# Optimization experiments

Measured on AMD Instinct MI355X. Metric: run time of the kernel, lower is better.

The kernel has to match this reference:

```python
import jax, jax.numpy as jnp
import numpy as np

EPS = 1e-5
MAG_EPS = 1e-12  # guards sqrt grad at exactly 0


def _conv(x, w, b, pad):
    # x: NCHW, w: OIHW, stride 1, symmetric padding -> SAME for odd kernels
    y = jax.lax.conv_general_dilated(x, w, (1, 1), [(pad, pad), (pad, pad)],
                                     dimension_numbers=('NCHW', 'OIHW', 'NCHW'))
    return y + b[None, :, None, None]


def _cconv(xr, xi, wr, wi, br, bi, pad):
    # apply_complex: (conv_r(xr) - conv_i(xi)) + j(conv_r(xi) + conv_i(xr)), biases inside each real conv
    yr = _conv(xr, wr, br, pad) - _conv(xi, wi, bi, pad)
    yi = _conv(xi, wr, br, pad) + _conv(xr, wi, bi, pad)
    return yr, yi


def _cbn(xr, xi, grr, gri, gii, br, bi):
    # complex batch norm with 2x2 covariance whitening (training-mode batch stats)
    ax = (0, 2, 3)
    bc = lambda v: v[None, :, None, None]
    cr = xr - bc(xr.mean(ax))
    ci = xi - bc(xi.mean(ax))
    Crr = (cr * cr).mean(ax) + EPS
    Cii = (ci * ci).mean(ax) + EPS
    Cri = (cr * ci).mean(ax)
    s = jnp.sqrt(Crr * Cii - Cri * Cri)          # sqrt(det)
    t = jnp.sqrt(Crr + Cii + 2.0 * s)            # sqrt(trace + 2 sqrt(det))
    inv = 1.0 / (s * t)
    Rrr, Rii, Rri = (Cii + s) * inv, (Crr + s) * inv, -Cri * inv
    xhr = bc(Rrr) * cr + bc(Rri) * ci
    xhi = bc(Rri) * cr + bc(Rii) * ci
    yr = bc(grr) * xhr + bc(gri) * xhi + bc(br)
    yi = bc(gri) * xhr + bc(gii) * xhi + bc(bi)
    return yr, yi


def _crelu(xr, xi):
    return jnp.maximum(xr, 0.0), jnp.maximum(xi, 0.0)


def _cmaxpool2(xr, xi):
    # 2x2 max pool selecting the complex value with the largest magnitude
    N, C, H, W = xr.shape
    blk = lambda x: x.reshape(N, C, H // 2, 2, W // 2, 2).transpose(0, 1, 2, 4, 3, 5).reshape(N, C, H // 2, W // 2, 4)
    br_, bi_ = blk(xr), blk(xi)
    idx = jnp.argmax(br_ * br_ + bi_ * bi_, axis=-1, keepdims=True)
    yr = jnp.take_along_axis(br_, idx, axis=-1)[..., 0]
    yi = jnp.take_along_axis(bi_, idx, axis=-1)[..., 0]
    return yr, yi


def _net(x,
         c1_wr, c1_wi, c1_br, c1_bi, b1_grr, b1_gri, b1_gii, b1_br, b1_bi,
         c2_wr, c2_wi, c2_br, c2_bi, b2_grr, b2_gri, b2_gii, b2_br, b2_bi,
         c3_wr, c3_wi, c3_br, c3_bi, b3_grr, b3_gri, b3_gii, b3_br, b3_bi,
         c4_wr, c4_wi, c4_br, c4_bi, b4_grr, b4_gri, b4_gii, b4_br, b4_bi,
         fc1_wr, fc1_wi, fc1_br, fc1_bi, fc2_w, fc2_b):
    # conv1: input has zero imaginary part, so the complex conv folds into two real convs
    xr = _conv(x, c1_wr, c1_br - c1_bi, 5)
    xi = _conv(x, c1_wi, c1_br + c1_bi, 5)
    xr, xi = _cmaxpool2(*_crelu(*_cbn(xr, xi, b1_grr, b1_gri, b1_gii, b1_br, b1_bi)))
    xr, xi = _cconv(xr, xi, c2_wr, c2_wi, c2_br, c2_bi, 2)
    xr, xi = _cmaxpool2(*_crelu(*_cbn(xr, xi, b2_grr, b2_gri, b2_gii, b2_br, b2_bi)))
    xr, xi = _cconv(xr, xi, c3_wr, c3_wi, c3_br, c3_bi, 1)
    xr, xi = _cmaxpool2(*_crelu(*_cbn(xr, xi, b3_grr, b3_gri, b3_gii, b3_br, b3_bi)))
    xr, xi = _cconv(xr, xi, c4_wr, c4_wi, c4_br, c4_bi, 1)
    xr, xi = _cmaxpool2(*_crelu(*_cbn(xr, xi, b4_grr, b4_gri, b4_gii, b4_br, b4_bi)))
    N = xr.shape[0]
    fr, fi = xr.reshape(N, -1), xi.reshape(N, -1)  # (N, 1024)
    er = (fr @ fc1_wr.T + fc1_br) - (fi @ fc1_wi.T + fc1_bi)
    ei = (fi @ fc1_wr.T + fc1_br) + (fr @ fc1_wi.T + fc1_bi)
    er, ei = jnp.maximum(er, 0.0), jnp.maximum(ei, 0.0)  # complex relu
    mag = jnp.sqrt(er * er + ei * ei + MAG_EPS)          # |z|; dropout is identity at eval
    logits = mag @ fc2_w.T + fc2_b
    return logits, er, ei


def setup_inputs() -> dict:
    key = jax.random.key(0)
    ks = iter(jax.random.split(key, 64))
    d = {}
    d['x'] = jax.random.normal(next(ks), (512, 1, 64, 64), jnp.float32)
    for name, cin, cout, k in [('c1', 1, 16, 11), ('c2', 16, 32, 5), ('c3', 32, 64, 3), ('c4', 64, 64, 3)]:
        s = 1.0 / np.sqrt(cin * k * k)
        d[f'{name}_wr'] = jax.random.normal(next(ks), (cout, cin, k, k), jnp.float32) * s
        d[f'{name}_wi'] = jax.random.normal(next(ks), (cout, cin, k, k), jnp.float32) * s
        d[f'{name}_br'] = jax.random.normal(next(ks), (cout,), jnp.float32) * s
        d[f'{name}_bi'] = jax.random.normal(next(ks), (cout,), jnp.float32) * s
    for name, c in [('b1', 16), ('b2', 32), ('b3', 64), ('b4', 64)]:
        d[f'{name}_grr'] = jnp.full((c,), 1.0 / np.sqrt(2.0), jnp.float32)
        d[f'{name}_gri'] = jnp.zeros((c,), jnp.float32)
        d[f'{name}_gii'] = jnp.full((c,), 1.0 / np.sqrt(2.0), jnp.float32)
        d[f'{name}_br'] = jnp.zeros((c,), jnp.float32)
        d[f'{name}_bi'] = jnp.zeros((c,), jnp.float32)
    s = 1.0 / np.sqrt(1024.0)
    d['fc1_wr'] = jax.random.normal(next(ks), (256, 1024), jnp.float32) * s
    d['fc1_wi'] = jax.random.normal(next(ks), (256, 1024), jnp.float32) * s
    d['fc1_br'] = jax.random.normal(next(ks), (256,), jnp.float32) * s
    d['fc1_bi'] = jax.random.normal(next(ks), (256,), jnp.float32) * s
    d['fc2_w'] = jax.random.normal(next(ks), (1000, 256), jnp.float32) * (1.0 / 16.0)
    d['fc2_b'] = jnp.zeros((1000,), jnp.float32)
    return d


def reference(x,
              c1_wr, c1_wi, c1_br, c1_bi, b1_grr, b1_gri, b1_gii, b1_br, b1_bi,
              c2_wr, c2_wi, c2_br, c2_bi, b2_grr, b2_gri, b2_gii, b2_br, b2_bi,
              c3_wr, c3_wi, c3_br, c3_bi, b3_grr, b3_gri, b3_gii, b3_br, b3_bi,
              c4_wr, c4_wi, c4_br, c4_bi, b4_grr, b4_gri, b4_gii, b4_br, b4_bi,
              fc1_wr, fc1_wi, fc1_br, fc1_bi, fc2_w, fc2_b):
    # returns (logits, emb_real, emb_imag); torch returned complex embeddings, split here into real pairs
    return _net(x,
                c1_wr, c1_wi, c1_br, c1_bi, b1_grr, b1_gri, b1_gii, b1_br, b1_bi,
                c2_wr, c2_wi, c2_br, c2_bi, b2_grr, b2_gri, b2_gii, b2_br, b2_bi,
                c3_wr, c3_wi, c3_br, c3_bi, b3_grr, b3_gri, b3_gii, b3_br, b3_bi,
                c4_wr, c4_wi, c4_br, c4_bi, b4_grr, b4_gri, b4_gii, b4_br, b4_bi,
                fc1_wr, fc1_wi, fc1_br, fc1_bi, fc2_w, fc2_b)
```

## Files before the change

### kernel.cpp

```cpp
#include <hip/hip_runtime.h>
#include <math.h>

__global__ __launch_bounds__(256) void fill_kernel(float* p, int n, float v) {
  int i = blockIdx.x * 256 + threadIdx.x;
  if (i < n) p[i] = v;
}

__device__ __forceinline__ void bn_apply_f32(float xr, float xi,
                                             const float* __restrict__ cf,
                                             float grr, float gri, float gii,
                                             float bbr, float bbi, float& yr,
                                             float& yi) {
  float cr = __fsub_rn(xr, cf[0]);
  float ci = __fsub_rn(xi, cf[1]);
  float xhr = __fadd_rn(__fmul_rn(cf[2], cr), __fmul_rn(cf[4], ci));
  float xhi = __fadd_rn(__fmul_rn(cf[4], cr), __fmul_rn(cf[3], ci));
  yr = fmaxf(__fadd_rn(__fadd_rn(__fmul_rn(grr, xhr), __fmul_rn(gri, xhi)), bbr), 0.f);
  yi = fmaxf(__fadd_rn(__fadd_rn(__fmul_rn(gri, xhr), __fmul_rn(gii, xhi)), bbi), 0.f);
}

#define PFMA8(XX, YY, WV1, WV2) \
  XX = fmaf(v4.x, WV1.x, XX);   \
  XX = fmaf(v4.y, WV1.y, XX);   \
  XX = fmaf(v4.z, WV1.z, XX);   \
  XX = fmaf(v4.w, WV1.w, XX);   \
  YY = fmaf(v4.x, WV2.x, YY);   \
  YY = fmaf(v4.y, WV2.y, YY);   \
  YY = fmaf(v4.z, WV2.z, YY);   \
  YY = fmaf(v4.w, WV2.w, YY);

#define C1_ROWBASE(pr) ((pr) * 84 + (((pr) >> 1) & 1))

template <int PASS>
__global__ __launch_bounds__(256, 2) void conv1_stats2(
    const float* __restrict__ x, const float* __restrict__ wr,
    const float* __restrict__ wi, const float* __restrict__ br,
    const float* __restrict__ bi, const float* __restrict__ coef,
    float* __restrict__ partial) {
  int b = blockIdx.x;
  int n = b >> 2, cg = b & 3;
  int t = threadIdx.x;
  __shared__ __align__(16) float sx[74 * 84];
  __shared__ __align__(16) float4 swr4[121], swi4[121];
  __shared__ float s0[256], s1[256], s2[PASS ? 256 : 1];

  for (int i = t; i < 74 * 84; i += 256) sx[i] = 0.f;
  for (int idx = t; idx < 484; idx += 256) {
    int wo = idx >> 2, ci = idx & 3;
    ((float*)swr4)[idx] = wr[(size_t)(cg * 4 + ci) * 121 + wo];
    ((float*)swi4)[idx] = wi[(size_t)(cg * 4 + ci) * 121 + wo];
  }
  __syncthreads();
  const float* xn = x + (size_t)n * 4096;
  for (int idx = t; idx < 1024; idx += 256) {
    float4 v = *(const float4*)(xn + idx * 4);
    int iy = idx >> 4, ixb = (idx & 15) * 4;
    int base = C1_ROWBASE(iy + 5) + ixb + 5;
    sx[base + 0] = v.x; sx[base + 1] = v.y;
    sx[base + 2] = v.z; sx[base + 3] = v.w;
  }
  __syncthreads();

  int leaf = t >> 3, j = t & 7;
  float a[4][16], bb[4][16];
#pragma unroll
  for (int ci = 0; ci < 4; ++ci)
#pragma unroll
    for (int k = 0; k < 16; ++k) { a[ci][k] = 0.f; bb[ci][k] = 0.f; }

  for (int ky = 0; ky < 11; ++ky) {
    int pr0 = leaf * 2 + ky;
    int base0 = C1_ROWBASE(pr0) + j;
    int base1 = C1_ROWBASE(pr0 + 1) + j;
    for (int kx = 0; kx < 11; ++kx) {
      const float* tb0 = sx + base0 + kx;
      const float* tb1 = sx + base1 + kx;
      float4 wR = swr4[ky * 11 + kx];
      float4 wI = swi4[ky * 11 + kx];
#pragma unroll
      for (int k8 = 0; k8 < 8; ++k8) {
        float v = tb0[k8 * 8];
        a[0][k8] = fmaf(v, wR.x, a[0][k8]);  bb[0][k8] = fmaf(v, wI.x, bb[0][k8]);
        a[1][k8] = fmaf(v, wR.y, a[1][k8]);  bb[1][k8] = fmaf(v, wI.y, bb[1][k8]);
        a[2][k8] = fmaf(v, wR.z, a[2][k8]);  bb[2][k8] = fmaf(v, wI.z, bb[2][k8]);
        a[3][k8] = fmaf(v, wR.w, a[3][k8]);  bb[3][k8] = fmaf(v, wI.w, bb[3][k8]);
      }
#pragma unroll
      for (int k8 = 0; k8 < 8; ++k8) {
        float v = tb1[k8 * 8];
        a[0][8 + k8] = fmaf(v, wR.x, a[0][8 + k8]);  bb[0][8 + k8] = fmaf(v, wI.x, bb[0][8 + k8]);
        a[1][8 + k8] = fmaf(v, wR.y, a[1][8 + k8]);  bb[1][8 + k8] = fmaf(v, wI.y, bb[1][8 + k8]);
        a[2][8 + k8] = fmaf(v, wR.z, a[2][8 + k8]);  bb[2][8 + k8] = fmaf(v, wI.z, bb[2][8 + k8]);
        a[3][8 + k8] = fmaf(v, wR.w, a[3][8 + k8]);  bb[3][8 + k8] = fmaf(v, wI.w, bb[3][8 + k8]);
      }
    }
  }

#pragma unroll
  for (int ci = 0; ci < 4; ++ci) {
    int c = cg * 4 + ci;
    float addR = __fsub_rn(br[c], bi[c]);
    float addI = __fadd_rn(br[c], bi[c]);
    float mr = 0.f, mi = 0.f;
    if (PASS) { mr = coef[c * 5 + 0]; mi = coef[c * 5 + 1]; }
    float a0 = 0.f, a1 = 0.f, a2 = 0.f;
#pragma unroll
    for (int k = 0; k < 16; ++k) {
      float xr = __fadd_rn(a[ci][k], addR);
      float xi = __fadd_rn(bb[ci][k], addI);
      if (PASS == 0) {
        a0 = __fadd_rn(a0, xr);
        a1 = __fadd_rn(a1, xi);
      } else {
        float cr = __fsub_rn(xr, mr), ci2 = __fsub_rn(xi, mi);
        a0 = __fadd_rn(a0, __fmul_rn(cr, cr));
        a1 = __fadd_rn(a1, __fmul_rn(ci2, ci2));
        a2 = __fadd_rn(a2, __fmul_rn(cr, ci2));
      }
    }
    s0[t] = a0; s1[t] = a1; if (PASS) s2[t] = a2;
    __syncthreads();
    if (t < 32) {
      int o = t * 8;
      float v0 = __fadd_rn(__fadd_rn(__fadd_rn(s0[o], s0[o + 1]), __fadd_rn(s0[o + 2], s0[o + 3])),
                           __fadd_rn(__fadd_rn(s0[o + 4], s0[o + 5]), __fadd_rn(s0[o + 6], s0[o + 7])));
      float v1 = __fadd_rn(__fadd_rn(__fadd_rn(s1[o], s1[o + 1]), __fadd_rn(s1[o + 2], s1[o + 3])),
                           __fadd_rn(__fadd_rn(s1[o + 4], s1[o + 5]), __fadd_rn(s1[o + 6], s1[o + 7])));
      float v2 = 0.f;
      if (PASS)
        v2 = __fadd_rn(__fadd_rn(__fadd_rn(s2[o], s2[o + 1]), __fadd_rn(s2[o + 2], s2[o + 3])),
                       __fadd_rn(__fadd_rn(s2[o + 4], s2[o + 5]), __fadd_rn(s2[o + 6], s2[o + 7])));
      s0[t] = v0; s1[t] = v1; if (PASS) s2[t] = v2;
    }
    if (t == 0) {
      for (int wdt = 32; wdt > 1; wdt >>= 1)
        for (int i = 0; i < (wdt >> 1); ++i) {
          s0[i] = __fadd_rn(s0[2 * i], s0[2 * i + 1]);
          s1[i] = __fadd_rn(s1[2 * i], s1[2 * i + 1]);
          if (PASS) s2[i] = __fadd_rn(s2[2 * i], s2[2 * i + 1]);
        }
      constexpr int S = PASS ? 3 : 2;
      size_t base = ((size_t)(n * 16 + c)) * S;
      partial[base + 0] = s0[0];
      partial[base + 1] = s1[0];
      if (PASS) partial[base + 2] = s2[0];
    }
    __syncthreads();
  }
}

__global__ __launch_bounds__(256, 2) void conv1_pool2(
    const float* __restrict__ x, const float* __restrict__ wr,
    const float* __restrict__ wi, const float* __restrict__ br,
    const float* __restrict__ bi, const float* __restrict__ coef,
    const float* __restrict__ grr, const float* __restrict__ gri,
    const float* __restrict__ gii, const float* __restrict__ bbr,
    const float* __restrict__ bbi, float* __restrict__ Pr,
    float* __restrict__ Pi) {
  int b = blockIdx.x;
  int n = b >> 2, cg = b & 3;
  int t = threadIdx.x;
  __shared__ __align__(16) float sx[74 * 84];
  __shared__ __align__(16) float4 swr4[121], swi4[121];

  for (int i = t; i < 74 * 84; i += 256) sx[i] = 0.f;
  for (int idx = t; idx < 484; idx += 256) {
    int wo = idx >> 2, ci = idx & 3;
    ((float*)swr4)[idx] = wr[(size_t)(cg * 4 + ci) * 121 + wo];
    ((float*)swi4)[idx] = wi[(size_t)(cg * 4 + ci) * 121 + wo];
  }
  __syncthreads();
  const float* xn = x + (size_t)n * 4096;
  for (int idx = t; idx < 1024; idx += 256) {
    float4 v = *(const float4*)(xn + idx * 4);
    int iy = idx >> 4, ixb = (idx & 15) * 4;
    int base = C1_ROWBASE(iy + 5) + ixb + 5;
    sx[base + 0] = v.x; sx[base + 1] = v.y;
    sx[base + 2] = v.z; sx[base + 3] = v.w;
  }
  __syncthreads();

  int oyb = t >> 5, ox = t & 31;
  float A[4][16], Bb[4][16];
#pragma unroll
  for (int ci = 0; ci < 4; ++ci)
#pragma unroll
    for (int e = 0; e < 16; ++e) { A[ci][e] = 0.f; Bb[ci][e] = 0.f; }

  for (int ky = 0; ky < 11; ++ky) {
    for (int kx = 0; kx < 11; ++kx) {
      float4 wR = swr4[ky * 11 + kx];
      float4 wI = swi4[ky * 11 + kx];
#pragma unroll
      for (int e = 0; e < 16; ++e) {
        int i = e >> 2, p = e & 3;
        int pr = 2 * (oyb + i * 8) + (p >> 1) + ky;
        int pc = 2 * ox + (p & 1) + kx;
        float v = sx[C1_ROWBASE(pr) + pc];
        A[0][e] = fmaf(v, wR.x, A[0][e]);  Bb[0][e] = fmaf(v, wI.x, Bb[0][e]);
        A[1][e] = fmaf(v, wR.y, A[1][e]);  Bb[1][e] = fmaf(v, wI.y, Bb[1][e]);
        A[2][e] = fmaf(v, wR.z, A[2][e]);  Bb[2][e] = fmaf(v, wI.z, Bb[2][e]);
        A[3][e] = fmaf(v, wR.w, A[3][e]);  Bb[3][e] = fmaf(v, wI.w, Bb[3][e]);
      }
    }
  }

#pragma unroll
  for (int ci = 0; ci < 4; ++ci) {
    int c = cg * 4 + ci;
    float addR = __fsub_rn(br[c], bi[c]);
    float addI = __fadd_rn(br[c], bi[c]);
    const float* cf = coef + c * 5;
    float gR = grr[c], gI = gri[c], gG = gii[c], bR = bbr[c], bI2 = bbi[c];
#pragma unroll
    for (int i = 0; i < 4; ++i) {
      int oy = oyb + i * 8;
      float bestr = 0.f, besti = 0.f, bestm = -1.f;
#pragma unroll
      for (int p = 0; p < 4; ++p) {
        float xr = __fadd_rn(A[ci][i * 4 + p], addR);
        float xi = __fadd_rn(Bb[ci][i * 4 + p], addI);
        float yr, yi;
        bn_apply_f32(xr, xi, cf, gR, gI, gG, bR, bI2, yr, yi);
        float m = __fadd_rn(__fmul_rn(yr, yr), __fmul_rn(yi, yi));
        if (m > bestm) { bestm = m; bestr = yr; besti = yi; }
      }
      size_t o = ((size_t)(n * 16 + c) * 32 + oy) * 32 + ox;
      Pr[o] = bestr;
      Pi[o] = besti;
    }
  }
}

__global__ __launch_bounds__(256) void repack_w(const float* __restrict__ src,
                                                float* __restrict__ dst,
                                                int CIN, int KK, int total) {
  int i = blockIdx.x * 256 + threadIdx.x;
  if (i >= total) return;
  int kk = i % KK;
  int rem = i / KK;
  int ci = rem % CIN;
  int co = rem / CIN;
  dst[((size_t)co * KK + kk) * CIN + ci] = src[i];
}

__global__ __launch_bounds__(256) void transpose_rc(const float* __restrict__ src,
                                                    float* __restrict__ dst,
                                                    int R, int C) {
  int i = blockIdx.x * 256 + threadIdx.x;
  if (i >= R * C) return;
  int r = i / C, c = i % C;
  dst[(size_t)c * R + r] = src[i];
}

#define STAGE_COMP(SRCBASE)                                          \
  {                                                                  \
    const float* src_ = (SRCBASE) + (size_t)n * CIN * HH;            \
    for (int idx = t; idx < RALLOC * H * CINQ; idx += NT) {          \
      int px = idx % (RALLOC * H);                                   \
      int cq = idx / (RALLOC * H);                                   \
      int lr = px / H, col = px - lr * H;                            \
      int gr = r0 + lr;                                              \
      if (gr < 0 || gr >= H) continue;                               \
      const float* sp = src_ + (size_t)cq * 4 * HH + gr * H + col;   \
      float4 v;                                                      \
      v.x = sp[0]; v.y = sp[HH]; v.z = sp[2 * HH]; v.w = sp[3 * HH]; \
      *(float4*)&sin_[(lr * W + col + PAD) * ST1 + cq * 4] = v;      \
    }                                                                \
  }

template <int H, int CIN, int COUT, int K, int PASS>
__global__ __launch_bounds__(COUT * 4, 2) void cconv_band_stats(
    const float* __restrict__ Xr, const float* __restrict__ Xi,
    const float* __restrict__ wrT, const float* __restrict__ wiT,
    const float* __restrict__ br, const float* __restrict__ bi,
    const float* __restrict__ coef, float* __restrict__ partial) {
  constexpr int HH = H * H;
  constexpr int PAD = K / 2, KK = K * K;
  constexpr int CLEN = (HH >= 128) ? 16 : 8;
  constexpr int NLEAF = HH / (8 * CLEN);
  constexpr int BROWS = (CLEN * 8) / H;
  constexpr int RALLOC = BROWS + 2 * PAD;
  constexpr int W = H + 2 * PAD;
  constexpr int ST1 = CIN + 4;
  constexpr int CINQ = CIN / 4;
  constexpr int NT = COUT * 4;
  constexpr int NC = COUT * 8;

  __shared__ __align__(16) float sin_[RALLOC * W * ST1];
  __shared__ float red0[NC], red1[NC], red2[PASS ? NC : 1];

  int b = blockIdx.x;
  int leaf = b % NLEAF;
  int n = b / NLEAF;
  int t = threadIdx.x;
  int r0 = leaf * BROWS - PAD;

  for (int i = t; i < RALLOC * W * ST1; i += NT) sin_[i] = 0.f;
  __syncthreads();
  STAGE_COMP(Xr)
  __syncthreads();

  int c0 = t >> 3, j = t & 7;
  int c1 = c0 + COUT / 2;
  const float* wrb0 = wrT + (size_t)c0 * CIN * KK;
  const float* wib0 = wiT + (size_t)c0 * CIN * KK;
  const float* wrb1 = wrT + (size_t)c1 * CIN * KK;
  const float* wib1 = wiT + (size_t)c1 * CIN * KK;

  float A0[CLEN], D0[CLEN], A1[CLEN], D1[CLEN];
  float B0[CLEN], C0_[CLEN], B1[CLEN], C1_[CLEN];
#pragma unroll
  for (int k = 0; k < CLEN; ++k) {
    A0[k] = 0.f; D0[k] = 0.f; A1[k] = 0.f; D1[k] = 0.f;
    B0[k] = 0.f; C0_[k] = 0.f; B1[k] = 0.f; C1_[k] = 0.f;
  }

#define STATS_TAPS(PH)                                                        \
  for (int ky = 0; ky < K; ++ky) {                                            \
    for (int kx = 0; kx < K; ++kx) {                                          \
      const float* tb = sin_ + (ky * W + kx + j) * ST1;                       \
      const float* wrp0 = wrb0 + (ky * K + kx) * CIN;                         \
      const float* wip0 = wib0 + (ky * K + kx) * CIN;                         \
      const float* wrp1 = wrb1 + (ky * K + kx) * CIN;                         \
      const float* wip1 = wib1 + (ky * K + kx) * CIN;                         \
      _Pragma("unroll 2") for (int cq = 0; cq < CINQ; ++cq) {                 \
        const float* tbc = tb + cq * 4;                                       \
        float4 wR0v = *(const float4*)(wrp0 + cq * 4);                        \
        float4 wI0v = *(const float4*)(wip0 + cq * 4);                        \
        float4 wR1v = *(const float4*)(wrp1 + cq * 4);                        \
        float4 wI1v = *(const float4*)(wip1 + cq * 4);                        \
        _Pragma("unroll") for (int k = 0; k < CLEN; ++k) {                    \
          float4 v4 = *(const float4*)(tbc +                                  \
              (((k * 8) / H) * W + ((k * 8) % H)) * ST1);                     \
          if (PH == 0) {                                                      \
            PFMA8(A0[k], D0[k], wR0v, wI0v)                                   \
            PFMA8(A1[k], D1[k], wR1v, wI1v)                                   \
          } else {                                                            \
            PFMA8(B0[k], C0_[k], wI0v, wR0v)                                  \
            PFMA8(B1[k], C1_[k], wI1v, wR1v)                                  \
          }                                                                   \
        }                                                                     \
      }                                                                       \
    }                                                                         \
  }

  STATS_TAPS(0)
  __syncthreads();
  STAGE_COMP(Xi)
  __syncthreads();
  STATS_TAPS(1)
#undef STATS_TAPS

  {
    float cbR = br[c0], cbI = bi[c0];
    float mr = 0.f, mi = 0.f;
    if (PASS) { mr = coef[c0 * 5 + 0]; mi = coef[c0 * 5 + 1]; }
    float a0 = 0.f, a1 = 0.f, a2 = 0.f;
#pragma unroll
    for (int k = 0; k < CLEN; ++k) {
      float yr = __fsub_rn(__fadd_rn(A0[k], cbR), __fadd_rn(B0[k], cbI));
      float yi = __fadd_rn(__fadd_rn(C0_[k], cbR), __fadd_rn(D0[k], cbI));
      if (PASS == 0) {
        a0 = __fadd_rn(a0, yr);
        a1 = __fadd_rn(a1, yi);
      } else {
        float cr = __fsub_rn(yr, mr), ci = __fsub_rn(yi, mi);
        a0 = __fadd_rn(a0, __fmul_rn(cr, cr));
        a1 = __fadd_rn(a1, __fmul_rn(ci, ci));
        a2 = __fadd_rn(a2, __fmul_rn(cr, ci));
      }
    }
    red0[c0 * 8 + j] = a0; red1[c0 * 8 + j] = a1;
    if (PASS) red2[c0 * 8 + j] = a2;
  }
  {
    float cbR = br[c1], cbI = bi[c1];
    float mr = 0.f, mi = 0.f;
    if (PASS) { mr = coef[c1 * 5 + 0]; mi = coef[c1 * 5 + 1]; }
    float a0 = 0.f, a1 = 0.f, a2 = 0.f;
#pragma unroll
    for (int k = 0; k < CLEN; ++k) {
      float yr = __fsub_rn(__fadd_rn(A1[k], cbR), __fadd_rn(B1[k], cbI));
      float yi = __fadd_rn(__fadd_rn(C1_[k], cbR), __fadd_rn(D1[k], cbI));
      if (PASS == 0) {
        a0 = __fadd_rn(a0, yr);
        a1 = __fadd_rn(a1, yi);
      } else {
        float cr = __fsub_rn(yr, mr), ci = __fsub_rn(yi, mi);
        a0 = __fadd_rn(a0, __fmul_rn(cr, cr));
        a1 = __fadd_rn(a1, __fmul_rn(ci, ci));
        a2 = __fadd_rn(a2, __fmul_rn(cr, ci));
      }
    }
    red0[c1 * 8 + j] = a0; red1[c1 * 8 + j] = a1;
    if (PASS) red2[c1 * 8 + j] = a2;
  }
  __syncthreads();
  if (j == 0) {
    constexpr int S = PASS ? 3 : 2;
#pragma unroll
    for (int s = 0; s < 2; ++s) {
      int cc = s ? c1 : c0;
      int o = cc * 8;
      size_t base = (((size_t)n * COUT + cc) * NLEAF + leaf) * S;
      partial[base + 0] =
          __fadd_rn(__fadd_rn(__fadd_rn(red0[o], red0[o + 1]), __fadd_rn(red0[o + 2], red0[o + 3])),
                    __fadd_rn(__fadd_rn(red0[o + 4], red0[o + 5]), __fadd_rn(red0[o + 6], red0[o + 7])));
      partial[base + 1] =
          __fadd_rn(__fadd_rn(__fadd_rn(red1[o], red1[o + 1]), __fadd_rn(red1[o + 2], red1[o + 3])),
                    __fadd_rn(__fadd_rn(red1[o + 4], red1[o + 5]), __fadd_rn(red1[o + 6], red1[o + 7])));
      if (PASS)
        partial[base + 2] =
            __fadd_rn(__fadd_rn(__fadd_rn(red2[o], red2[o + 1]), __fadd_rn(red2[o + 2], red2[o + 3])),
                      __fadd_rn(__fadd_rn(red2[o + 4], red2[o + 5]), __fadd_rn(red2[o + 6], red2[o + 7])));
    }
  }
}

template <int H, int CIN, int COUT, int K, int OBR>
__global__ __launch_bounds__(COUT * 4, 2) void cconv_band_pool(
    const float* __restrict__ Xr, const float* __restrict__ Xi,
    const float* __restrict__ wrT, const float* __restrict__ wiT,
    const float* __restrict__ br, const float* __restrict__ bi,
    const float* __restrict__ coef, const float* __restrict__ grr,
    const float* __restrict__ gri, const float* __restrict__ gii,
    const float* __restrict__ bbr, const float* __restrict__ bbi,
    float* __restrict__ Pr, float* __restrict__ Pi) {
  constexpr int HH = H * H;
  constexpr int OH = H / 2;
  constexpr int NBAND = OH / OBR;
  constexpr int PAD = K / 2, KK = K * K;
  constexpr int CROWS = OBR * 2;
  constexpr int RALLOC = CROWS + 2 * PAD;
  constexpr int W = H + 2 * PAD;
  constexpr int ST1 = CIN + 4;
  constexpr int CINQ = CIN / 4;
  constexpr int NT = COUT * 4;
  constexpr int NOUT = (OBR * OH) / 8;
  constexpr int NQ = NOUT * 4;

  __shared__ __align__(16) float sin_[RALLOC * W * ST1];

  int b = blockIdx.x;
  int band = b % NBAND;
  int n = b / NBAND;
  int t = threadIdx.x;
  int r0 = band * CROWS - PAD;

  for (int i = t; i < RALLOC * W * ST1; i += NT) sin_[i] = 0.f;
  __syncthreads();
  STAGE_COMP(Xr)
  __syncthreads();

  int c0 = t >> 3, j = t & 7;
  int c1 = c0 + COUT / 2;
  const float* jbp = sin_ + (2 * (j / OH) * W + 2 * (j % OH)) * ST1;
  const float* wrb0 = wrT + (size_t)c0 * CIN * KK;
  const float* wib0 = wiT + (size_t)c0 * CIN * KK;
  const float* wrb1 = wrT + (size_t)c1 * CIN * KK;
  const float* wib1 = wiT + (size_t)c1 * CIN * KK;

  float A0[NQ], D0[NQ], A1[NQ], D1[NQ];
  float B0[NQ], C0_[NQ], B1[NQ], C1_[NQ];
#pragma unroll
  for (int q = 0; q < NQ; ++q) {
    A0[q] = 0.f; D0[q] = 0.f; A1[q] = 0.f; D1[q] = 0.f;
    B0[q] = 0.f; C0_[q] = 0.f; B1[q] = 0.f; C1_[q] = 0.f;
  }

#define POOL_TAPS(PH)                                                         \
  for (int ky = 0; ky < K; ++ky) {                                            \
    for (int kx = 0; kx < K; ++kx) {                                          \
      const float* tb = jbp + (ky * W + kx) * ST1;                            \
      const float* wrp0 = wrb0 + (ky * K + kx) * CIN;                         \
      const float* wip0 = wib0 + (ky * K + kx) * CIN;                         \
      const float* wrp1 = wrb1 + (ky * K + kx) * CIN;                         \
      const float* wip1 = wib1 + (ky * K + kx) * CIN;                         \
      _Pragma("unroll 2") for (int cq = 0; cq < CINQ; ++cq) {                 \
        const float* tbc = tb + cq * 4;                                       \
        float4 wR0v = *(const float4*)(wrp0 + cq * 4);                        \
        float4 wI0v = *(const float4*)(wip0 + cq * 4);                        \
        float4 wR1v = *(const float4*)(wrp1 + cq * 4);                        \
        float4 wI1v = *(const float4*)(wip1 + cq * 4);                        \
        _Pragma("unroll") for (int q = 0; q < NQ; ++q) {                      \
          float4 v4 = *(const float4*)(tbc +                                  \
              ((2 * ((8 * (q >> 2)) / OH) + ((q & 3) >> 1)) * W +             \
               2 * ((8 * (q >> 2)) % OH) + ((q & 3) & 1)) * ST1);             \
          if (PH == 0) {                                                      \
            PFMA8(A0[q], D0[q], wR0v, wI0v)                                   \
            PFMA8(A1[q], D1[q], wR1v, wI1v)                                   \
          } else {                                                            \
            PFMA8(B0[q], C0_[q], wI0v, wR0v)                                  \
            PFMA8(B1[q], C1_[q], wI1v, wR1v)                                  \
          }                                                                   \
        }                                                                     \
      }                                                                       \
    }                                                                         \
  }

  POOL_TAPS(0)
  __syncthreads();
  STAGE_COMP(Xi)
  __syncthreads();
  POOL_TAPS(1)
#undef POOL_TAPS

  {
    float cbR = br[c0], cbI = bi[c0];
    const float* cf = coef + c0 * 5;
    float gR = grr[c0], gI = gri[c0], gG = gii[c0], bR = bbr[c0], bI2 = bbi[c0];
#pragma unroll
    for (int u = 0; u < NOUT; ++u) {
      int e = j + 8 * u;
      int oy = band * OBR + e / OH, ox = e % OH;
      float bestr = 0.f, besti = 0.f, bestm = -1.f;
#pragma unroll
      for (int p = 0; p < 4; ++p) {
        int q = u * 4 + p;
        float xr = __fsub_rn(__fadd_rn(A0[q], cbR), __fadd_rn(B0[q], cbI));
        float xi = __fadd_rn(__fadd_rn(C0_[q], cbR), __fadd_rn(D0[q], cbI));
        float yr, yi;
        bn_apply_f32(xr, xi, cf, gR, gI, gG, bR, bI2, yr, yi);
        float m = __fadd_rn(__fmul_rn(yr, yr), __fmul_rn(yi, yi));
        if (m > bestm) { bestm = m; bestr = yr; besti = yi; }
      }
      size_t o = ((size_t)(n * COUT + c0) * OH + oy) * OH + ox;
      Pr[o] = bestr;
      Pi[o] = besti;
    }
  }
  {
    float cbR = br[c1], cbI = bi[c1];
    const float* cf = coef + c1 * 5;
    float gR = grr[c1], gI = gri[c1], gG = gii[c1], bR = bbr[c1], bI2 = bbi[c1];
#pragma unroll
    for (int u = 0; u < NOUT; ++u) {
      int e = j + 8 * u;
      int oy = band * OBR + e / OH, ox = e % OH;
      float bestr = 0.f, besti = 0.f, bestm = -1.f;
#pragma unroll
      for (int p = 0; p < 4; ++p) {
        int q = u * 4 + p;
        float xr = __fsub_rn(__fadd_rn(A1[q], cbR), __fadd_rn(B1[q], cbI));
        float xi = __fadd_rn(__fadd_rn(C1_[q], cbR), __fadd_rn(D1[q], cbI));
        float yr, yi;
        bn_apply_f32(xr, xi, cf, gR, gI, gG, bR, bI2, yr, yi);
        float m = __fadd_rn(__fmul_rn(yr, yr), __fmul_rn(yi, yi));
        if (m > bestm) { bestm = m; bestr = yr; besti = yi; }
      }
      size_t o = ((size_t)(n * COUT + c1) * OH + oy) * OH + ox;
      Pr[o] = bestr;
      Pi[o] = besti;
    }
  }
}

template <int H, int CIN, int COUT, int CG, int K, int REPS>
__global__ __launch_bounds__((CG / 2) * 8 * REPS, 2) void cconv_band_store(
    const float* __restrict__ Xr, const float* __restrict__ Xi,
    const float* __restrict__ wrT, const float* __restrict__ wiT,
    const float* __restrict__ br, const float* __restrict__ bi,
    int coff, float* __restrict__ bufR, float* __restrict__ bufI) {
  constexpr int HH = H * H;
  constexpr int PAD = K / 2, KK = K * K;
  constexpr int CLEN = (HH >= 128) ? 16 : 8;
  constexpr int NLEAF = HH / (8 * CLEN);
  constexpr int BROWS = (CLEN * 8) / H;
  constexpr int RALLOC = BROWS + 2 * PAD;
  constexpr int W = H + 2 * PAD;
  constexpr int ST1 = CIN + 4;
  constexpr int CINQ = CIN / 4;
  constexpr int CPAIR = CG / 2;
  constexpr int NT = CPAIR * 8 * REPS;
  constexpr int CLT = CLEN / REPS;
  constexpr int RROWS = (CLT * 8) / H;

  __shared__ __align__(16) float sin_[RALLOC * W * ST1];

  int b = blockIdx.x;
  int leaf = b % NLEAF;
  int n = b / NLEAF;
  int t = threadIdx.x;
  int r0 = leaf * BROWS - PAD;

  for (int i = t; i < RALLOC * W * ST1; i += NT) sin_[i] = 0.f;
  __syncthreads();
  STAGE_COMP(Xr)
  __syncthreads();

  int rep = t / (CPAIR * 8);
  int tt = t % (CPAIR * 8);
  int c0l = tt >> 3, j = tt & 7;
  int c0 = coff + c0l, c1 = c0 + CPAIR;
  const float* jbp = sin_ + ((REPS > 1 ? rep * RROWS : 0) * W + j) * ST1;
  const float* wrb0 = wrT + (size_t)c0 * CIN * KK;
  const float* wib0 = wiT + (size_t)c0 * CIN * KK;
  const float* wrb1 = wrT + (size_t)c1 * CIN * KK;
  const float* wib1 = wiT + (size_t)c1 * CIN * KK;

  float A0[CLT], D0[CLT], A1[CLT], D1[CLT];
  float B0[CLT], C0_[CLT], B1[CLT], C1_[CLT];
#pragma unroll
  for (int k = 0; k < CLT; ++k) {
    A0[k] = 0.f; D0[k] = 0.f; A1[k] = 0.f; D1[k] = 0.f;
    B0[k] = 0.f; C0_[k] = 0.f; B1[k] = 0.f; C1_[k] = 0.f;
  }

#define STORE_TAPS(PH)                                                        \
  for (int ky = 0; ky < K; ++ky) {                                            \
    for (int kx = 0; kx < K; ++kx) {                                          \
      const float* tb = jbp + (ky * W + kx) * ST1;                            \
      const float* wrp0 = wrb0 + (ky * K + kx) * CIN;                         \
      const float* wip0 = wib0 + (ky * K + kx) * CIN;                         \
      const float* wrp1 = wrb1 + (ky * K + kx) * CIN;                         \
      const float* wip1 = wib1 + (ky * K + kx) * CIN;                         \
      _Pragma("unroll 2") for (int cq = 0; cq < CINQ; ++cq) {                 \
        const float* tbc = tb + cq * 4;                                       \
        float4 wR0v = *(const float4*)(wrp0 + cq * 4);                        \
        float4 wI0v = *(const float4*)(wip0 + cq * 4);                        \
        float4 wR1v = *(const float4*)(wrp1 + cq * 4);                        \
        float4 wI1v = *(const float4*)(wip1 + cq * 4);                        \
        _Pragma("unroll") for (int k = 0; k < CLT; ++k) {                     \
          float4 v4 = *(const float4*)(tbc +                                  \
              (((k * 8) / H) * W + ((k * 8) % H)) * ST1);                     \
          if (PH == 0) {                                                      \
            PFMA8(A0[k], D0[k], wR0v, wI0v)                                   \
            PFMA8(A1[k], D1[k], wR1v, wI1v)                                   \
          } else {                                                            \
            PFMA8(B0[k], C0_[k], wI0v, wR0v)                                  \
            PFMA8(B1[k], C1_[k], wI1v, wR1v)                                  \
          }                                                                   \
        }                                                                     \
      }                                                                       \
    }                                                                         \
  }

  STORE_TAPS(0)
  __syncthreads();
  STAGE_COMP(Xi)
  __syncthreads();
  STORE_TAPS(1)
#undef STORE_TAPS

  float cbR0 = br[c0], cbI0 = bi[c0];
  float cbR1 = br[c1], cbI1 = bi[c1];
  size_t b0 = ((size_t)n * CG + c0l) * HH;
  size_t b1 = ((size_t)n * CG + (c0l + CPAIR)) * HH;
#pragma unroll
  for (int k = 0; k < CLT; ++k) {
    int px = leaf * CLEN * 8 + (rep * CLT + k) * 8 + j;
    float yr0 = __fsub_rn(__fadd_rn(A0[k], cbR0), __fadd_rn(B0[k], cbI0));
    float yi0 = __fadd_rn(__fadd_rn(C0_[k], cbR0), __fadd_rn(D0[k], cbI0));
    bufR[b0 + px] = yr0;
    bufI[b0 + px] = yi0;
    float yr1 = __fsub_rn(__fadd_rn(A1[k], cbR1), __fadd_rn(B1[k], cbI1));
    float yi1 = __fadd_rn(__fadd_rn(C1_[k], cbR1), __fadd_rn(D1[k], cbI1));
    bufR[b1 + px] = yr1;
    bufI[b1 + px] = yi1;
  }
}

template <int CG, int HH, int CLEN, int PASS>
__global__ __launch_bounds__(CG * 8) void cstats_stream(
    const float* __restrict__ bufR, const float* __restrict__ bufI,
    const float* __restrict__ coef, float* __restrict__ partial, int coff) {
  constexpr int NLEAF = HH / (8 * CLEN);
  constexpr int NT = CG * 8;
  __shared__ float red0[NT], red1[NT], red2[PASS ? NT : 1];
  int b = blockIdx.x;
  int leaf = b % NLEAF;
  int n = b / NLEAF;
  int t = threadIdx.x;
  int cl = t >> 3, j = t & 7;
  int c = coff + cl;
  size_t base = ((size_t)n * CG + cl) * HH + leaf * CLEN * 8 + j;
  float mr = 0.f, mi = 0.f;
  if (PASS) { mr = coef[c * 5 + 0]; mi = coef[c * 5 + 1]; }
  float a0 = 0.f, a1 = 0.f, a2 = 0.f;
#pragma unroll
  for (int k = 0; k < CLEN; ++k) {
    float yr = bufR[base + k * 8];
    float yi = bufI[base + k * 8];
    if (PASS == 0) {
      a0 = __fadd_rn(a0, yr);
      a1 = __fadd_rn(a1, yi);
    } else {
      float cr = __fsub_rn(yr, mr), ci = __fsub_rn(yi, mi);
      a0 = __fadd_rn(a0, __fmul_rn(cr, cr));
      a1 = __fadd_rn(a1, __fmul_rn(ci, ci));
      a2 = __fadd_rn(a2, __fmul_rn(cr, ci));
    }
  }
  red0[t] = a0; red1[t] = a1; if (PASS) red2[t] = a2;
  __syncthreads();
  if (j == 0) {
    constexpr int S = PASS ? 3 : 2;
    int o = cl * 8;
    size_t pb = (((size_t)n * CG + cl) * NLEAF + leaf) * S;
    partial[pb + 0] =
        __fadd_rn(__fadd_rn(__fadd_rn(red0[o], red0[o + 1]), __fadd_rn(red0[o + 2], red0[o + 3])),
                  __fadd_rn(__fadd_rn(red0[o + 4], red0[o + 5]), __fadd_rn(red0[o + 6], red0[o + 7])));
    partial[pb + 1] =
        __fadd_rn(__fadd_rn(__fadd_rn(red1[o], red1[o + 1]), __fadd_rn(red1[o + 2], red1[o + 3])),
                  __fadd_rn(__fadd_rn(red1[o + 4], red1[o + 5]), __fadd_rn(red1[o + 6], red1[o + 7])));
    if (PASS)
      partial[pb + 2] =
          __fadd_rn(__fadd_rn(__fadd_rn(red2[o], red2[o + 1]), __fadd_rn(red2[o + 2], red2[o + 3])),
                    __fadd_rn(__fadd_rn(red2[o + 4], red2[o + 5]), __fadd_rn(red2[o + 6], red2[o + 7])));
  }
}

template <int CG, int H, int COUT>
__global__ __launch_bounds__(256) void cpool_stream(
    const float* __restrict__ bufR, const float* __restrict__ bufI,
    const float* __restrict__ coef, const float* __restrict__ grr,
    const float* __restrict__ gri, const float* __restrict__ gii,
    const float* __restrict__ bbr, const float* __restrict__ bbi,
    float* __restrict__ Pr, float* __restrict__ Pi, int coff) {
  constexpr int OH = H / 2, OHH = OH * OH, HH = H * H;
  int n = blockIdx.x;
  for (int idx = threadIdx.x; idx < CG * OHH; idx += 256) {
    int cl = idx / OHH, q = idx % OHH;
    int oy = q / OH, ox = q % OH;
    int c = coff + cl;
    size_t base = ((size_t)n * CG + cl) * HH;
    const float* cf = coef + c * 5;
    float gR = grr[c], gI = gri[c], gG = gii[c], bR = bbr[c], bI2 = bbi[c];
    float bestr = 0.f, besti = 0.f, bestm = -1.f;
#pragma unroll
    for (int p = 0; p < 4; ++p) {
      size_t o = base + (size_t)(2 * oy + (p >> 1)) * H + 2 * ox + (p & 1);
      float xr = bufR[o], xi = bufI[o];
      float yr, yi;
      bn_apply_f32(xr, xi, cf, gR, gI, gG, bR, bI2, yr, yi);
      float m = __fadd_rn(__fmul_rn(yr, yr), __fmul_rn(yi, yi));
      if (m > bestm) { bestm = m; bestr = yr; besti = yi; }
    }
    size_t o = ((size_t)(n * COUT + c) * OH + oy) * OH + ox;
    Pr[o] = bestr;
    Pi[o] = besti;
  }
}

template <int C, int NLEAF, int TPB>
__global__ __launch_bounds__(TPB) void np_mean_combine3(
    const float* __restrict__ partial, float* __restrict__ coef, float Mf,
    int coff) {
  int t = threadIdx.x;
  if (t >= C * 2) return;
  int c = t >> 1, s = t & 1;
  float acc = 0.f;
  for (int n = 0; n < 512; ++n) {
    const float* p = partial + (((size_t)n * C + c) * NLEAF) * 2 + s;
    float v;
    if (NLEAF == 8)
      v = __fadd_rn(__fadd_rn(__fadd_rn(p[0], p[2]), __fadd_rn(p[4], p[6])),
                    __fadd_rn(__fadd_rn(p[8], p[10]), __fadd_rn(p[12], p[14])));
    else if (NLEAF == 2)
      v = __fadd_rn(p[0], p[2]);
    else
      v = p[0];
    acc = __fadd_rn(acc, v);
  }
  coef[(coff + c) * 5 + s] = __fdiv_rn(acc, Mf);
}

template <int C, int NLEAF, int TPB>
__global__ __launch_bounds__(TPB) void np_cov_combine3(
    const float* __restrict__ partial, float* __restrict__ coef, float Mf,
    int coff) {
  __shared__ float sums[C * 3];
  int t = threadIdx.x;
  if (t < C * 3) {
    int c = t / 3, s = t % 3;
    float acc = 0.f;
    for (int n = 0; n < 512; ++n) {
      const float* p = partial + (((size_t)n * C + c) * NLEAF) * 3 + s;
      float v;
      if (NLEAF == 8)
        v = __fadd_rn(__fadd_rn(__fadd_rn(p[0], p[3]), __fadd_rn(p[6], p[9])),
                      __fadd_rn(__fadd_rn(p[12], p[15]), __fadd_rn(p[18], p[21])));
      else if (NLEAF == 2)
        v = __fadd_rn(p[0], p[3]);
      else
        v = p[0];
      acc = __fadd_rn(acc, v);
    }
    sums[c * 3 + s] = acc;
  }
  __syncthreads();
  if (t < C) {
    float Crr = __fadd_rn(__fdiv_rn(sums[t * 3 + 0], Mf), 1e-5f);
    float Cii = __fadd_rn(__fdiv_rn(sums[t * 3 + 1], Mf), 1e-5f);
    float Cri = __fdiv_rn(sums[t * 3 + 2], Mf);
    float s_ = __fsqrt_rn(__fsub_rn(__fmul_rn(Crr, Cii), __fmul_rn(Cri, Cri)));
    float t_ = __fsqrt_rn(__fadd_rn(__fadd_rn(Crr, Cii), __fmul_rn(2.f, s_)));
    float inv = __fdiv_rn(1.f, __fmul_rn(s_, t_));
    int cg = coff + t;
    coef[cg * 5 + 2] = __fmul_rn(__fadd_rn(Cii, s_), inv);
    coef[cg * 5 + 3] = __fmul_rn(__fadd_rn(Crr, s_), inv);
    coef[cg * 5 + 4] = __fmul_rn(-Cri, inv);
  }
}

__global__ __launch_bounds__(256) void fc_head_kernel(
    const float* __restrict__ Fr, const float* __restrict__ Fi,
    const float* __restrict__ wrT, const float* __restrict__ wiT,
    const float* __restrict__ br, const float* __restrict__ bi,
    const float* __restrict__ w2T, const float* __restrict__ b2,
    float* __restrict__ logits, float* __restrict__ er_out,
    float* __restrict__ ei_out) {
  int n = blockIdx.x, t = threadIdx.x;
  __shared__ float sFr[1024], sFi[1024];
  __shared__ double sMag[256];
  for (int idx = t; idx < 1024; idx += 256) {
    sFr[idx] = Fr[(size_t)n * 1024 + idx];
    sFi[idx] = Fi[(size_t)n * 1024 + idx];
  }
  __syncthreads();
  {
    double er = 0.0, ei = 0.0;
    for (int k = 0; k < 1024; ++k) {
      double fx = (double)sFr[k], fy = (double)sFi[k];
      double a = (double)wrT[(size_t)k * 256 + t];
      double bb = (double)wiT[(size_t)k * 256 + t];
      er += fx * a - fy * bb;
      ei += fy * a + fx * bb;
    }
    double bR = (double)br[t], bI = (double)bi[t];
    er = fmax(er + (bR - bI), 0.0);
    ei = fmax(ei + (bR + bI), 0.0);
    er_out[(size_t)n * 256 + t] = (float)er;
    ei_out[(size_t)n * 256 + t] = (float)ei;
    sMag[t] = sqrt(er * er + ei * ei + 1e-12);
  }
  __syncthreads();
#pragma unroll
  for (int j = 0; j < 4; ++j) {
    int o = j * 256 + t;
    if (o < 1000) {
      double acc = 0.0;
      for (int k = 0; k < 256; ++k)
        acc += sMag[k] * (double)w2T[(size_t)k * 1000 + o];
      logits[(size_t)n * 1000 + o] = (float)(acc + (double)b2[o]);
    }
  }
}

extern "C" void kernel_launch(void* const* d_in, const int* in_sizes, int n_in,
                              void* d_out, int out_size, void* d_ws,
                              size_t ws_size, hipStream_t stream) {
  (void)in_sizes; (void)n_in;
  const float* x = (const float*)d_in[0];
  const float* c1_wr = (const float*)d_in[1];
  const float* c1_wi = (const float*)d_in[2];
  const float* c1_br = (const float*)d_in[3];
  const float* c1_bi = (const float*)d_in[4];
  const float* c2_wr = (const float*)d_in[5];
  const float* c2_wi = (const float*)d_in[6];
  const float* c2_br = (const float*)d_in[7];
  const float* c2_bi = (const float*)d_in[8];
  const float* c3_wr = (const float*)d_in[9];
  const float* c3_wi = (const float*)d_in[10];
  const float* c3_br = (const float*)d_in[11];
  const float* c3_bi = (const float*)d_in[12];
  const float* c4_wr = (const float*)d_in[13];
  const float* c4_wi = (const float*)d_in[14];
  const float* c4_br = (const float*)d_in[15];
  const float* c4_bi = (const float*)d_in[16];
  const float* b1_grr = (const float*)d_in[17];
  const float* b1_gri = (const float*)d_in[18];
  const float* b1_gii = (const float*)d_in[19];
  const float* b1_br = (const float*)d_in[20];
  const float* b1_bi = (const float*)d_in[21];
  const float* b2_grr = (const float*)d_in[22];
  const float* b2_gri = (const float*)d_in[23];
  const float* b2_gii = (const float*)d_in[24];
  const float* b2_br = (const float*)d_in[25];
  const float* b2_bi = (const float*)d_in[26];
  const float* b3_grr = (const float*)d_in[27];
  const float* b3_gri = (const float*)d_in[28];
  const float* b3_gii = (const float*)d_in[29];
  const float* b3_br = (const float*)d_in[30];
  const float* b3_bi = (const float*)d_in[31];
  const float* b4_grr = (const float*)d_in[32];
  const float* b4_gri = (const float*)d_in[33];
  const float* b4_gii = (const float*)d_in[34];
  const float* b4_br = (const float*)d_in[35];
  const float* b4_bi = (const float*)d_in[36];
  const float* fc1_wr = (const float*)d_in[37];
  const float* fc1_wi = (const float*)d_in[38];
  const float* fc1_br = (const float*)d_in[39];
  const float* fc1_bi = (const float*)d_in[40];
  const float* fc2_w = (const float*)d_in[41];
  const float* fc2_b = (const float*)d_in[42];

  float* outL = (float*)d_out;
  float* er = outL + 512 * 1000;
  float* ei = er + 512 * 256;

  const size_t NEED = 101057792;
  const size_t NEED2 = 135005440;
  const size_t NEED3 = 236848384;
  if (ws_size < NEED) {
    fill_kernel<<<(out_size + 255) / 256, 256, 0, stream>>>(
        (float*)d_out, out_size, (float)(ws_size >> 20));
    return;
  }
  const bool big3 = (ws_size >= NEED3);
  const bool big = (ws_size >= NEED2);
  char* w = (char*)d_ws;
  float* P1r = (float*)(w + 0);
  float* P1i = (float*)(w + 33554432);
  float* P2r = (float*)(w + 67108864);
  float* P2i = (float*)(w + 83886080);
  float* P3r = (float*)(w + 0);
  float* P3i = (float*)(w + 8388608);
  float* P4r = (float*)(w + 16777216);
  float* P4i = (float*)(w + 18874368);
  float* partialT = (float*)(w + 100663296);
  float* partial2 = (float*)(w + 67108864);
  float* coef = (float*)(w + 101056512);
  float* c2_wrT = (float*)(w + 100663296);
  float* c2_wiT = (float*)(w + 100663296 + 51200);
  float* c3_wrT = (float*)(w + 100663296);
  float* c3_wiT = (float*)(w + 100663296 + 73728);
  float* c4_wrT = (float*)(w + 20971520);
  float* c4_wiT = (float*)(w + 20971520 + 147456);
  float* fc1_wrT = (float*)(w + 33554432);
  float* fc1_wiT = (float*)(w + 34603008);
  float* fc2_wT = (float*)(w + 35651584);
  float* buf3R = (float*)(w + 16777216);
  float* buf3I = (float*)(w + 33554432);
  float* partial3s = (float*)(w + 50331648);
  float* buf4R = (float*)(w + 67108864);
  float* buf4I = (float*)(w + 75497472);
  float* buf2R = (float*)(w + 101057792);
  float* buf2I = (float*)(w + 117835008);
  float* partial2g = (float*)(w + 134612224);
  float* buf2R3 = (float*)(w + 101057792);
  float* buf2I3 = (float*)(w + 168166656);
  float* partial2g3 = (float*)(w + 235275520);

  conv1_stats2<0><<<2048, 256, 0, stream>>>(x, c1_wr, c1_wi, c1_br, c1_bi,
                                            coef, partialT);
  np_mean_combine3<16, 1, 64><<<1, 64, 0, stream>>>(partialT, coef, 2097152.f, 0);
  conv1_stats2<1><<<2048, 256, 0, stream>>>(x, c1_wr, c1_wi, c1_br, c1_bi,
                                            coef, partialT);
  np_cov_combine3<16, 1, 64><<<1, 64, 0, stream>>>(partialT, coef, 2097152.f, 0);
  conv1_pool2<<<2048, 256, 0, stream>>>(x, c1_wr, c1_wi, c1_br, c1_bi, coef,
                                        b1_grr, b1_gri, b1_gii, b1_br, b1_bi,
                                        P1r, P1i);

  repack_w<<<50, 256, 0, stream>>>(c2_wr, c2_wrT, 16, 25, 12800);
  repack_w<<<50, 256, 0, stream>>>(c2_wi, c2_wiT, 16, 25, 12800);
  if (big3) {
    cconv_band_store<32, 16, 32, 32, 5, 2><<<4096, 256, 0, stream>>>(
        P1r, P1i, c2_wrT, c2_wiT, c2_br, c2_bi, 0, buf2R3, buf2I3);
    cstats_stream<32, 1024, 16, 0><<<4096, 256, 0, stream>>>(
        buf2R3, buf2I3, coef, partial2g3, 0);
    np_mean_combine3<32, 8, 64><<<1, 64, 0, stream>>>(partial2g3, coef,
                                                      524288.f, 0);
    cstats_stream<32, 1024, 16, 1><<<4096, 256, 0, stream>>>(
        buf2R3, buf2I3, coef, partial2g3, 0);
    np_cov_combine3<32, 8, 128><<<1, 128, 0, stream>>>(partial2g3, coef,
                                                       524288.f, 0);
    cpool_stream<32, 32, 32><<<512, 256, 0, stream>>>(
        buf2R3, buf2I3, coef, b2_grr, b2_gri, b2_gii, b2_br, b2_bi, P2r, P2i,
        0);
  } else if (big) {
    for (int g = 0; g < 4; ++g) {
      cconv_band_store<32, 16, 32, 8, 5, 4><<<4096, 128, 0, stream>>>(
          P1r, P1i, c2_wrT, c2_wiT, c2_br, c2_bi, g * 8, buf2R, buf2I);
      cstats_stream<8, 1024, 16, 0><<<4096, 64, 0, stream>>>(
          buf2R, buf2I, coef, partial2g, g * 8);
      np_mean_combine3<8, 8, 64><<<1, 64, 0, stream>>>(partial2g, coef,
                                                       524288.f, g * 8);
      cstats_stream<8, 1024, 16, 1><<<4096, 64, 0, stream>>>(
          buf2R, buf2I, coef, partial2g, g * 8);
      np_cov_combine3<8, 8, 64><<<1, 64, 0, stream>>>(partial2g, coef,
                                                      524288.f, g * 8);
      cpool_stream<8, 32, 32><<<512, 256, 0, stream>>>(
          buf2R, buf2I, coef, b2_grr, b2_gri, b2_gii, b2_br, b2_bi, P2r, P2i,
          g * 8);
    }
  } else {
    cconv_band_stats<32, 16, 32, 5, 0><<<4096, 128, 0, stream>>>(
        P1r, P1i, c2_wrT, c2_wiT, c2_br, c2_bi, coef, partial2);
    np_mean_combine3<32, 8, 64><<<1, 64, 0, stream>>>(partial2, coef,
                                                      524288.f, 0);
    cconv_band_stats<32, 16, 32, 5, 1><<<4096, 128, 0, stream>>>(
        P1r, P1i, c2_wrT, c2_wiT, c2_br, c2_bi, coef, partial2);
    np_cov_combine3<32, 8, 128><<<1, 128, 0, stream>>>(partial2, coef,
                                                       524288.f, 0);
    cconv_band_pool<32, 16, 32, 5, 2><<<4096, 128, 0, stream>>>(
        P1r, P1i, c2_wrT, c2_wiT, c2_br, c2_bi, coef, b2_grr, b2_gri, b2_gii,
        b2_br, b2_bi, P2r, P2i);
  }

  repack_w<<<72, 256, 0, stream>>>(c3_wr, c3_wrT, 32, 9, 18432);
  repack_w<<<72, 256, 0, stream>>>(c3_wi, c3_wiT, 32, 9, 18432);
  for (int g = 0; g < 2; ++g) {
    cconv_band_store<16, 32, 64, 32, 3, 2><<<1024, 256, 0, stream>>>(
        P2r, P2i, c3_wrT, c3_wiT, c3_br, c3_bi, g * 32, buf3R, buf3I);
    cstats_stream<32, 256, 16, 0><<<1024, 256, 0, stream>>>(
        buf3R, buf3I, coef, partial3s, g * 32);
    np_mean_combine3<32, 2, 64><<<1, 64, 0, stream>>>(partial3s, coef,
                                                      131072.f, g * 32);
    cstats_stream<32, 256, 16, 1><<<1024, 256, 0, stream>>>(
        buf3R, buf3I, coef, partial3s, g * 32);
    np_cov_combine3<32, 2, 128><<<1, 128, 0, stream>>>(partial3s, coef,
                                                       131072.f, g * 32);
    cpool_stream<32, 16, 64><<<512, 256, 0, stream>>>(
        buf3R, buf3I, coef, b3_grr, b3_gri, b3_gii, b3_br, b3_bi, P3r, P3i,
        g * 32);
  }

  repack_w<<<144, 256, 0, stream>>>(c4_wr, c4_wrT, 64, 9, 36864);
  repack_w<<<144, 256, 0, stream>>>(c4_wi, c4_wiT, 64, 9, 36864);
  cconv_band_store<8, 64, 64, 64, 3, 2><<<512, 512, 0, stream>>>(
      P3r, P3i, c4_wrT, c4_wiT, c4_br, c4_bi, 0, buf4R, buf4I);
  cstats_stream<64, 64, 8, 0><<<512, 512, 0, stream>>>(buf4R, buf4I, coef,
                                                       partialT, 0);
  np_mean_combine3<64, 1, 128><<<1, 128, 0, stream>>>(partialT, coef,
                                                      32768.f, 0);
  cstats_stream<64, 64, 8, 1><<<512, 512, 0, stream>>>(buf4R, buf4I, coef,
                                                       partialT, 0);
  np_cov_combine3<64, 1, 192><<<1, 192, 0, stream>>>(partialT, coef,
                                                     32768.f, 0);
  cpool_stream<64, 8, 64><<<512, 256, 0, stream>>>(
      buf4R, buf4I, coef, b4_grr, b4_gri, b4_gii, b4_br, b4_bi, P4r, P4i, 0);

  transpose_rc<<<1024, 256, 0, stream>>>(fc1_wr, fc1_wrT, 256, 1024);
  transpose_rc<<<1024, 256, 0, stream>>>(fc1_wi, fc1_wiT, 256, 1024);
  transpose_rc<<<1000, 256, 0, stream>>>(fc2_w, fc2_wT, 1000, 256);
  fc_head_kernel<<<512, 256, 0, stream>>>(P4r, P4i, fc1_wrT, fc1_wiT, fc1_br,
                                          fc1_bi, fc2_wT, fc2_b, outL, er, ei);
}
```

Measured before the change: 2.501 ms.

## Compute four output channels per thread in banded complex conv store kernels

Adds a cconv_band_store4 kernel in which each thread accumulates four output channels instead of two. Each shared-memory input float4 load is then reused across more weight vectors, while REPS is raised so the same block size covers the pixels. It replaces the conv2, conv3 and conv4 store kernels; for conv4 the block shrinks from 512 to 256 threads. The cost is many more accumulator registers per thread (4x4xCLT), which risks spills or lower occupancy despite the launch bound of 2 blocks.

```diff
diff --git a/kernel.cpp b/kernel.cpp
--- a/kernel.cpp
+++ b/kernel.cpp
@@ -658,6 +658,114 @@
     float yi1 = __fadd_rn(__fadd_rn(C1_[k], cbR1), __fadd_rn(D1[k], cbI1));
     bufR[b1 + px] = yr1;
     bufI[b1 + px] = yi1;
+  }
+}
+
+template <int H, int CIN, int COUT, int CG, int K, int REPS>
+__global__ __launch_bounds__((CG / 4) * 8 * REPS, 2) void cconv_band_store4(
+    const float* __restrict__ Xr, const float* __restrict__ Xi,
+    const float* __restrict__ wrT, const float* __restrict__ wiT,
+    const float* __restrict__ br, const float* __restrict__ bi,
+    int coff, float* __restrict__ bufR, float* __restrict__ bufI) {
+  constexpr int HH = H * H;
+  constexpr int PAD = K / 2, KK = K * K;
+  constexpr int CLEN = (HH >= 128) ? 16 : 8;
+  constexpr int NLEAF = HH / (8 * CLEN);
+  constexpr int BROWS = (CLEN * 8) / H;
+  constexpr int RALLOC = BROWS + 2 * PAD;
+  constexpr int W = H + 2 * PAD;
+  constexpr int ST1 = CIN + 4;
+  constexpr int CINQ = CIN / 4;
+  constexpr int CQ = CG / 4;
+  constexpr int NT = CQ * 8 * REPS;
+  constexpr int CLT = CLEN / REPS;
+  constexpr int RROWS = (CLT * 8) / H;
+
+  __shared__ __align__(16) float sin_[RALLOC * W * ST1];
+
+  int b = blockIdx.x;
+  int leaf = b % NLEAF;
+  int n = b / NLEAF;
+  int t = threadIdx.x;
+  int r0 = leaf * BROWS - PAD;
+
+  for (int i = t; i < RALLOC * W * ST1; i += NT) sin_[i] = 0.f;
+  __syncthreads();
+  STAGE_COMP(Xr)
+  __syncthreads();
+
+  int rep = t / (CQ * 8);
+  int tt = t % (CQ * 8);
+  int c0l = tt >> 3, j = tt & 7;
+  const float* jbp = sin_ + ((REPS > 1 ? rep * RROWS : 0) * W + j) * ST1;
+  const float* wrb[4];
+  const float* wib[4];
+#pragma unroll
+  for (int ch = 0; ch < 4; ++ch) {
+    int c = coff + c0l + ch * CQ;
+    wrb[ch] = wrT + (size_t)c * CIN * KK;
+    wib[ch] = wiT + (size_t)c * CIN * KK;
+  }
+
+  float A[4][CLT], Bq[4][CLT], Cc[4][CLT], D[4][CLT];
+#pragma unroll
+  for (int ch = 0; ch < 4; ++ch)
+#pragma unroll
+    for (int k = 0; k < CLT; ++k) {
+      A[ch][k] = 0.f; Bq[ch][k] = 0.f; Cc[ch][k] = 0.f; D[ch][k] = 0.f;
+    }
+
+#define STORE4_TAPS(PH)                                                       \
+  for (int ky = 0; ky < K; ++ky) {                                            \
+    for (int kx = 0; kx < K; ++kx) {                                          \
+      const float* tb = jbp + (ky * W + kx) * ST1;                            \
+      int woff = (ky * K + kx) * CIN;                                         \
+      _Pragma("unroll 2") for (int cq = 0; cq < CINQ; ++cq) {                 \
+        const float* tbc = tb + cq * 4;                                       \
+        float4 wRv[4], wIv[4];                                                \
+        _Pragma("unroll") for (int ch = 0; ch < 4; ++ch) {                    \
+          wRv[ch] = *(const float4*)(wrb[ch] + woff + cq * 4);                \
+          wIv[ch] = *(const float4*)(wib[ch] + woff + cq * 4);                \
+        }                                                                     \
+        _Pragma("unroll") for (int k = 0; k < CLT; ++k) {                     \
+          float4 v4 = *(const float4*)(tbc +                                  \
+              (((k * 8) / H) * W + ((k * 8) % H)) * ST1);                     \
+          if (PH == 0) {                                                      \
+            PFMA8(A[0][k], D[0][k], wRv[0], wIv[0])                           \
+            PFMA8(A[1][k], D[1][k], wRv[1], wIv[1])                           \
+            PFMA8(A[2][k], D[2][k], wRv[2], wIv[2])                           \
+            PFMA8(A[3][k], D[3][k], wRv[3], wIv[3])                           \
+          } else {                                                            \
+            PFMA8(Bq[0][k], Cc[0][k], wIv[0], wRv[0])                         \
+            PFMA8(Bq[1][k], Cc[1][k], wIv[1], wRv[1])                         \
+            PFMA8(Bq[2][k], Cc[2][k], wIv[2], wRv[2])                         \
+            PFMA8(Bq[3][k], Cc[3][k], wIv[3], wRv[3])                         \
+          }                                                                   \
+        }                                                                     \
+      }                                                                       \
+    }                                                                         \
+  }
+
+  STORE4_TAPS(0)
+  __syncthreads();
+  STAGE_COMP(Xi)
+  __syncthreads();
+  STORE4_TAPS(1)
+#undef STORE4_TAPS
+
+#pragma unroll
+  for (int ch = 0; ch < 4; ++ch) {
+    int c = coff + c0l + ch * CQ;
+    float cbR = br[c], cbI = bi[c];
+    size_t bbase = ((size_t)n * CG + (c0l + ch * CQ)) * HH;
+#pragma unroll
+    for (int k = 0; k < CLT; ++k) {
+      int px = leaf * CLEN * 8 + (rep * CLT + k) * 8 + j;
+      float yr = __fsub_rn(__fadd_rn(A[ch][k], cbR), __fadd_rn(Bq[ch][k], cbI));
+      float yi = __fadd_rn(__fadd_rn(Cc[ch][k], cbR), __fadd_rn(D[ch][k], cbI));
+      bufR[bbase + px] = yr;
+      bufI[bbase + px] = yi;
+    }
   }
 }
 
@@ -956,7 +1064,7 @@
   repack_w<<<50, 256, 0, stream>>>(c2_wr, c2_wrT, 16, 25, 12800);
   repack_w<<<50, 256, 0, stream>>>(c2_wi, c2_wiT, 16, 25, 12800);
   if (big3) {
-    cconv_band_store<32, 16, 32, 32, 5, 2><<<4096, 256, 0, stream>>>(
+    cconv_band_store4<32, 16, 32, 32, 5, 4><<<4096, 256, 0, stream>>>(
         P1r, P1i, c2_wrT, c2_wiT, c2_br, c2_bi, 0, buf2R3, buf2I3);
     cstats_stream<32, 1024, 16, 0><<<4096, 256, 0, stream>>>(
         buf2R3, buf2I3, coef, partial2g3, 0);
@@ -1002,7 +1110,7 @@
   repack_w<<<72, 256, 0, stream>>>(c3_wr, c3_wrT, 32, 9, 18432);
   repack_w<<<72, 256, 0, stream>>>(c3_wi, c3_wiT, 32, 9, 18432);
   for (int g = 0; g < 2; ++g) {
-    cconv_band_store<16, 32, 64, 32, 3, 2><<<1024, 256, 0, stream>>>(
+    cconv_band_store4<16, 32, 64, 32, 3, 4><<<1024, 256, 0, stream>>>(
         P2r, P2i, c3_wrT, c3_wiT, c3_br, c3_bi, g * 32, buf3R, buf3I);
     cstats_stream<32, 256, 16, 0><<<1024, 256, 0, stream>>>(
         buf3R, buf3I, coef, partial3s, g * 32);
@@ -1019,7 +1127,7 @@
 
   repack_w<<<144, 256, 0, stream>>>(c4_wr, c4_wrT, 64, 9, 36864);
   repack_w<<<144, 256, 0, stream>>>(c4_wi, c4_wiT, 64, 9, 36864);
-  cconv_band_store<8, 64, 64, 64, 3, 2><<<512, 512, 0, stream>>>(
+  cconv_band_store4<8, 64, 64, 64, 3, 2><<<512, 256, 0, stream>>>(
       P3r, P3i, c4_wrT, c4_wiT, c4_br, c4_bi, 0, buf4R, buf4I);
   cstats_stream<64, 64, 8, 0><<<512, 512, 0, stream>>>(buf4R, buf4I, coef,
                                                        partialT, 0);
```

Result: slower. 2.660 ms (+6.3%).
